# Kernel tuning notes

Measured on AMD Instinct MI355X. Metric: run time of the kernel, lower is better.

Reference implementation:

```python
import jax, jax.numpy as jnp
import numpy as np

B, C_IN, C_OUT, H, W = 32, 64, 128, 56, 56


def setup_inputs() -> dict:
    key = jax.random.key(0)
    k1, k2, k3 = jax.random.split(key, 3)
    x = jax.random.normal(k1, (B, C_IN, H, W), dtype=jnp.float32)
    # Original build(): kernel ~ N(0,1) in spatial domain, then fft2d; the
    # real/imag parts of the spectrum are the learned variables.
    kernel = jax.random.normal(k2, (C_OUT, C_IN, H, W), dtype=jnp.float32)
    kernel_fft = jnp.fft.fft2(kernel.astype(jnp.complex64))
    kernel_real = jnp.real(kernel_fft).astype(jnp.float32)
    kernel_imag = jnp.imag(kernel_fft).astype(jnp.float32)
    bias = jnp.zeros((C_OUT,), dtype=jnp.float32)
    return {"x": x, "kernel_real": kernel_real, "kernel_imag": kernel_imag, "bias": bias}


def reference(x, kernel_real, kernel_imag, bias):
    # FFT-based convolution, vectorized over batch (original used a per-batch
    # Python loop + concat; math is identical).
    x_fft = jnp.fft.fft2(x.astype(jnp.complex64))              # [B, Cin, H, W]
    kernel_freq = jax.lax.complex(kernel_real, kernel_imag)    # [Cout, Cin, H, W]
    # elementwise complex multiply + reduce over input channels
    y_fft = jnp.einsum('oihw,bihw->bohw', kernel_freq, x_fft)  # [B, Cout, H, W]
    y = jnp.real(jnp.fft.ifft2(y_fft))                         # [B, Cout, H, W]
    return y + bias[None, :, None, None]
```

## Files before the change

### kernel.cpp

```cpp
#include <hip/hip_runtime.h>


#define HH 56
#define NF 3136
#define KH 29
#define NFH 1624
constexpr int B = 32, CIN = 64, COUT = 128;
constexpr float PI2 = 6.283185307179586f;

typedef unsigned short u16;
typedef __attribute__((ext_vector_type(8))) short s8v;
typedef __attribute__((ext_vector_type(4))) float f4v;
typedef __attribute__((ext_vector_type(4))) int i4v;

#define MFMA(a, b, c) __builtin_amdgcn_mfma_f32_16x16x32_bf16(a, b, c, 0, 0, 0)

__device__ __host__ inline short f2bf(float f) {
    unsigned u = __builtin_bit_cast(unsigned, f);
    u += 0x7fffu + ((u >> 16) & 1u);
    return (short)(u >> 16);
}

__device__ inline unsigned pk2(float a, float b) {
    return (unsigned)(u16)f2bf(a) | ((unsigned)(u16)f2bf(b) << 16);
}

__device__ inline s8v negbf(s8v a) {
    i4v t = __builtin_bit_cast(i4v, a);
    t ^= (int)0x80008000u;
    return __builtin_bit_cast(s8v, t);
}

__global__ __launch_bounds__(256) void ksetup(short* __restrict__ cpool) {
    int i = blockIdx.x * 256 + threadIdx.x;
    if (i < 4608) {
        int m = i / 72, n = i % 72;
        float c = 0.f, s = 0.f;
        if (m < 56 && n < 56) {
            float ang = PI2 * (float)((m * n) % 56) / 56.f;
            c = cosf(ang); s = sinf(ang);
        }
        cpool[i]        = f2bf(c);
        cpool[4608 + i] = f2bf(s);
    } else if (i < 7168) {
        int j = i - 4608;
        int h = j / 40, kh = j % 40;
        float c = 0.f, s = 0.f;
        if (h < 56 && kh < 29) {
            float w = (kh == 0 || kh == 28) ? 1.f : 2.f;
            float ang = PI2 * (float)((h * kh) % 56) / 56.f;
            float sc = w * (1.f / 3136.f);
            c = sc * cosf(ang);
            s = -sc * sinf(ang);
        }
        cpool[13824 + j] = f2bf(c);
        cpool[16384 + j] = f2bf(s);
    }
}

__global__ __launch_bounds__(256) void kprep(const float* __restrict__ Kr,
                                             const float* __restrict__ Ki,
                                             u16* __restrict__ Kbr,
                                             u16* __restrict__ Kbi) {
    __shared__ __align__(8) u16 Lr[64 * 60], Li[64 * 60];
    const int tid = threadIdx.x;
    const int oi0 = blockIdx.x * 64;
    const int f0  = blockIdx.y * 56;
    for (int c = tid; c < 896; c += 256) {
        int row = c / 14, c4 = (c % 14) * 4;
        size_t g = (size_t)(oi0 + row) * NF + f0 + c4;
        float4 vr = *(const float4*)&Kr[g];
        float4 vi = *(const float4*)&Ki[g];
        *(uint2*)&Lr[row * 60 + c4] = make_uint2(pk2(vr.x, vr.y), pk2(vr.z, vr.w));
        *(uint2*)&Li[row * 60 + c4] = make_uint2(pk2(vi.x, vi.y), pk2(vi.z, vi.w));
    }
    __syncthreads();
    for (int idx = tid; idx < 896; idx += 256) {
        int c = idx & 15, f = idx >> 4;
        int j0 = c * 4;
        unsigned r01 = (unsigned)Lr[j0 * 60 + f]       | ((unsigned)Lr[(j0 + 1) * 60 + f] << 16);
        unsigned r23 = (unsigned)Lr[(j0 + 2) * 60 + f] | ((unsigned)Lr[(j0 + 3) * 60 + f] << 16);
        unsigned i01 = (unsigned)Li[j0 * 60 + f]       | ((unsigned)Li[(j0 + 1) * 60 + f] << 16);
        unsigned i23 = (unsigned)Li[(j0 + 2) * 60 + f] | ((unsigned)Li[(j0 + 3) * 60 + f] << 16);
        size_t o = (size_t)(f0 + f) * 8192 + oi0 + j0;
        *(uint2*)&Kbr[o] = make_uint2(r01, r23);
        *(uint2*)&Kbi[o] = make_uint2(i01, i23);
    }
}

__global__ __launch_bounds__(512) void kfwd(const float* __restrict__ x,
                                            const short* __restrict__ cpool,
                                            ushort2* __restrict__ Xb) {
    __shared__ __align__(16) short Cw[4608], Sw[4608];
    __shared__ __align__(16) short xs[2][4608];
    __shared__ __align__(16) short T1r[2][4608], T1i[2][4608];
    const int tid = threadIdx.x;
    {
        const int4* src = (const int4*)cpool;
        for (int i = tid; i < 576; i += 512) {
            ((int4*)Cw)[i] = src[i];
            ((int4*)Sw)[i] = src[576 + i];
        }
    }
    for (int i = tid; i < 4608; i += 512) ((int*)xs)[i] = 0;
    __syncthreads();
    const int half = tid >> 8, tid2 = tid & 255;
    const float* xp = x + (size_t)(blockIdx.x * 2 + half) * NF;
    short* xsh = xs[half];
    for (int c = tid2; c < 784; c += 256) {
        int r = c / 14, c4 = (c % 14) * 4;
        float4 v = *(const float4*)&xp[r * 56 + c4];
        *(uint2*)&xsh[r * 72 + c4] = make_uint2(pk2(v.x, v.y), pk2(v.z, v.w));
    }
    __syncthreads();

    const int lane = tid & 63;
    const int wv = tid >> 6;
    const int hw = wv >> 2;
    const int nt = wv & 3;
    const int q = lane >> 4, l15 = lane & 15;

    f4v aR[4] = {}, aI[4] = {};
    for (int ks = 0; ks < 2; ++ks) {
        const int bo = (nt * 16 + l15) * 72 + ks * 32 + q * 8;
        s8v bC  = *(const s8v*)&Cw[bo];
        s8v bSN = negbf(*(const s8v*)&Sw[bo]);
        for (int mt = 0; mt < 4; ++mt) {
            s8v a = *(const s8v*)&xs[hw][(mt * 16 + l15) * 72 + ks * 32 + q * 8];
            aR[mt] = MFMA(a, bC, aR[mt]);
            aI[mt] = MFMA(a, bSN, aI[mt]);
        }
    }
    for (int mt = 0; mt < 4; ++mt) {
        int o = (nt * 16 + l15) * 72 + mt * 16 + q * 4;
        *(uint2*)&T1r[hw][o] = make_uint2(pk2(aR[mt][0], aR[mt][1]),
                                          pk2(aR[mt][2], aR[mt][3]));
        *(uint2*)&T1i[hw][o] = make_uint2(pk2(aI[mt][0], aI[mt][1]),
                                          pk2(aI[mt][2], aI[mt][3]));
    }
    __syncthreads();

    f4v xr[2] = {}, xi2[2] = {};
    for (int ks = 0; ks < 2; ++ks) {
        const int bo = (nt * 16 + l15) * 72 + ks * 32 + q * 8;
        s8v br = *(const s8v*)&T1r[hw][bo];
        s8v bi = *(const s8v*)&T1i[hw][bo];
        for (int mt = 0; mt < 2; ++mt) {
            const int ao = (mt * 16 + l15) * 72 + ks * 32 + q * 8;
            s8v aC  = *(const s8v*)&Cw[ao];
            s8v aS  = *(const s8v*)&Sw[ao];
            s8v aSN = negbf(aS);
            xr[mt]  = MFMA(aC, br, xr[mt]);
            xr[mt]  = MFMA(aS, bi, xr[mt]);
            xi2[mt] = MFMA(aC, bi, xi2[mt]);
            xi2[mt] = MFMA(aSN, br, xi2[mt]);
        }
    }
    ushort2* op = Xb + (size_t)(blockIdx.x * 2 + hw) * NFH;
    const int kw = nt * 16 + l15;
    if (kw < 56) {
        for (int mt = 0; mt < 2; ++mt)
            for (int r = 0; r < 4; ++r) {
                int kh = mt * 16 + q * 4 + r;
                if (kh < 29)
                    op[kh * 56 + kw] = make_ushort2((u16)f2bf(xr[mt][r]),
                                                    (u16)f2bf(xi2[mt][r]));
            }
    }
}

__global__ __launch_bounds__(512) void kmix(const ushort2* __restrict__ Xb,
                                            const u16* __restrict__ Kbr,
                                            const u16* __restrict__ Kbi,
                                            ushort2* __restrict__ Yb) {
    __shared__ __align__(16) u16 Xr[8 * 2304], Xi[8 * 2304];
    const int tid = threadIdx.x;
    const int f0 = blockIdx.x * 8;

    for (int rr = 0; rr < 4; ++rr) {
        int row = rr * 512 + tid;
        const uint4* src = (const uint4*)(Xb + (size_t)row * NFH + f0);
        uint4 v0 = src[0], v1 = src[1];
        int base = (row >> 6) * 72 + (row & 63);
        unsigned uu[8] = {v0.x, v0.y, v0.z, v0.w, v1.x, v1.y, v1.z, v1.w};
        #pragma unroll
        for (int ff = 0; ff < 8; ++ff) {
            Xr[ff * 2304 + base] = (u16)uu[ff];
            Xi[ff * 2304 + base] = (u16)(uu[ff] >> 16);
        }
    }
    __syncthreads();

    const int lane = tid & 63;
    const int wv = tid >> 6;
    const int q = lane >> 4, l15 = lane & 15;

    unsigned pk[2][4][8];

    #pragma unroll
    for (int ff = 0; ff < 8; ++ff) {
        const int f = f0 + ff;
        const size_t kb = (size_t)f * 8192 + (size_t)(wv * 16 + l15) * 64 + q * 8;
        s8v bkr0 = *(const s8v*)&Kbr[kb];
        s8v bkr1 = *(const s8v*)&Kbr[kb + 32];
        s8v bki0 = *(const s8v*)&Kbi[kb];
        s8v bki1 = *(const s8v*)&Kbi[kb + 32];

        f4v yr[2] = {}, yi[2] = {};
        #pragma unroll
        for (int mt = 0; mt < 2; ++mt) {
            const int ao = ff * 2304 + (mt * 16 + l15) * 72 + q * 8;
            s8v axr0 = *(const s8v*)&Xr[ao];
            s8v axr1 = *(const s8v*)&Xr[ao + 32];
            s8v axi0 = *(const s8v*)&Xi[ao];
            s8v axi1 = *(const s8v*)&Xi[ao + 32];
            s8v axn0 = negbf(axi0), axn1 = negbf(axi1);
            yr[mt] = MFMA(axr0, bkr0, yr[mt]);
            yr[mt] = MFMA(axn0, bki0, yr[mt]);
            yr[mt] = MFMA(axr1, bkr1, yr[mt]);
            yr[mt] = MFMA(axn1, bki1, yr[mt]);
            yi[mt] = MFMA(axr0, bki0, yi[mt]);
            yi[mt] = MFMA(axi0, bkr0, yi[mt]);
            yi[mt] = MFMA(axr1, bki1, yi[mt]);
            yi[mt] = MFMA(axi1, bkr1, yi[mt]);
        }
        #pragma unroll
        for (int mt = 0; mt < 2; ++mt)
            #pragma unroll
            for (int r = 0; r < 4; ++r)
                pk[mt][r][ff] = (unsigned)(u16)f2bf(yr[mt][r]) |
                                ((unsigned)(u16)f2bf(yi[mt][r]) << 16);
    }

    const int o = wv * 16 + l15;
    #pragma unroll
    for (int mt = 0; mt < 2; ++mt)
        #pragma unroll
        for (int r = 0; r < 4; ++r) {
            const int b = mt * 16 + q * 4 + r;
            uint4* dst = (uint4*)(Yb + (size_t)(b * COUT + o) * NFH + f0);
            dst[0] = make_uint4(pk[mt][r][0], pk[mt][r][1],
                                pk[mt][r][2], pk[mt][r][3]);
            dst[1] = make_uint4(pk[mt][r][4], pk[mt][r][5],
                                pk[mt][r][6], pk[mt][r][7]);
        }
}

__global__ __launch_bounds__(512) void kinv(const ushort2* __restrict__ Yf,
                                            const short* __restrict__ cpool,
                                            const float* __restrict__ bias,
                                            float* __restrict__ out) {
    __shared__ __align__(16) short Cw[4608], Sw[4608];
    __shared__ __align__(16) short A2C[2560], A2S[2560];
    __shared__ __align__(16) short Yr[2][2304], Yi[2][2304];
    __shared__ __align__(16) short ZTr[2][2560], ZTi[2][2560];
    const int tid = threadIdx.x;
    {
        const int4* src = (const int4*)cpool;
        for (int i = tid; i < 576; i += 512) {
            ((int4*)Cw)[i] = src[i];
            ((int4*)Sw)[i] = src[576 + i];
        }
        for (int i = tid; i < 320; i += 512) {
            ((int4*)A2C)[i] = src[1728 + i];
            ((int4*)A2S)[i] = src[2048 + i];
        }
    }
    for (int i = tid; i < 2304; i += 512) { ((int*)Yr)[i] = 0; ((int*)Yi)[i] = 0; }
    __syncthreads();
    const int half = tid >> 8, tid2 = tid & 255;
    const ushort2* yp = Yf + (size_t)(blockIdx.x * 2 + half) * NFH;
    for (int c = tid2; c < 406; c += 256) {
        uint4 v = *(const uint4*)&yp[c * 4];
        int f = c * 4, kh = f / 56, kwb = f % 56;
        int o = kh * 72 + kwb;
        *(uint2*)&Yr[half][o] = make_uint2((v.x & 0xffffu) | (v.y << 16),
                                           (v.z & 0xffffu) | (v.w << 16));
        *(uint2*)&Yi[half][o] = make_uint2((v.x >> 16) | (v.y & 0xffff0000u),
                                           (v.z >> 16) | (v.w & 0xffff0000u));
    }
    __syncthreads();

    const int lane = tid & 63;
    const int wv = tid >> 6;
    const int hw = wv >> 2, nt = wv & 3;
    const int q = lane >> 4, l15 = lane & 15;

    f4v zr[2] = {}, zi[2] = {};
    for (int ks = 0; ks < 2; ++ks) {
        const int bo = (nt * 16 + l15) * 72 + ks * 32 + q * 8;
        s8v bC = *(const s8v*)&Cw[bo];
        s8v bS = *(const s8v*)&Sw[bo];
        for (int mt = 0; mt < 2; ++mt) {
            const int ao = (mt * 16 + l15) * 72 + ks * 32 + q * 8;
            s8v ar  = *(const s8v*)&Yr[hw][ao];
            s8v ai  = *(const s8v*)&Yi[hw][ao];
            s8v ain = negbf(ai);
            zr[mt] = MFMA(ar, bC, zr[mt]);
            zr[mt] = MFMA(ain, bS, zr[mt]);
            zi[mt] = MFMA(ar, bS, zi[mt]);
            zi[mt] = MFMA(ai, bC, zi[mt]);
        }
    }
    for (int mt = 0; mt < 2; ++mt) {
        int o = (nt * 16 + l15) * 40 + mt * 16 + q * 4;
        *(uint2*)&ZTr[hw][o] = make_uint2(pk2(zr[mt][0], zr[mt][1]),
                                          pk2(zr[mt][2], zr[mt][3]));
        *(uint2*)&ZTi[hw][o] = make_uint2(pk2(zi[mt][0], zi[mt][1]),
                                          pk2(zi[mt][2], zi[mt][3]));
    }
    __syncthreads();

    f4v yv[4] = {};
    {
        const int bo = (nt * 16 + l15) * 40 + q * 8;
        s8v br = *(const s8v*)&ZTr[hw][bo];
        s8v bi = *(const s8v*)&ZTi[hw][bo];
        for (int mt = 0; mt < 4; ++mt) {
            const int ao = (mt * 16 + l15) * 40 + q * 8;
            s8v ac  = *(const s8v*)&A2C[ao];
            s8v as_ = *(const s8v*)&A2S[ao];
            yv[mt] = MFMA(ac, br, yv[mt]);
            yv[mt] = MFMA(as_, bi, yv[mt]);
        }
    }
    const int img = blockIdx.x * 2 + hw;
    const float bv = bias[img & (COUT - 1)];
    float* opx = out + (size_t)img * NF;
    const int w = nt * 16 + l15;
    if (w < 56) {
        for (int mt = 0; mt < 4; ++mt)
            for (int r = 0; r < 4; ++r) {
                int h = mt * 16 + q * 4 + r;
                if (h < 56) opx[h * 56 + w] = yv[mt][r] + bv;
            }
    }
}

extern "C" void kernel_launch(void* const* d_in, const int* in_sizes, int n_in,
                              void* d_out, int out_size, void* d_ws, size_t ws_size,
                              hipStream_t stream) {
    const float* x    = (const float*)d_in[0];
    const float* Kr   = (const float*)d_in[1];
    const float* Ki   = (const float*)d_in[2];
    const float* bias = (const float*)d_in[3];

    short*   cpool = (short*)d_ws;
    ushort2* Xb  = (ushort2*)((char*)d_ws + 40960);
    ushort2* Yb  = (ushort2*)((char*)d_ws + 40960 + 13307904);
    u16*     Kbr = (u16*)((char*)d_ws + 40960 + 13307904 + 26615808);
    u16*     Kbi = Kbr + (size_t)13307904;

    hipLaunchKernelGGL(ksetup, dim3(28), dim3(256), 0, stream, cpool);
    hipLaunchKernelGGL(kprep, dim3(128, 29), dim3(256), 0, stream, Kr, Ki, Kbr, Kbi);
    hipLaunchKernelGGL(kfwd, dim3(B * CIN / 2), dim3(512), 0, stream, x, cpool, Xb);
    hipLaunchKernelGGL(kmix, dim3(NFH / 8), dim3(512), 0, stream, Xb, Kbr, Kbi, Yb);
    hipLaunchKernelGGL(kinv, dim3(B * COUT / 2), dim3(512), 0, stream,
                       Yb, cpool, bias, (float*)d_out);
}
```

Measured before the change: 305.4 us.

## Merge kernel prep and forward FFT into one launch; split mixing over output channels

Kernel-spectrum conversion and the forward DFT now run in a single launch, with block index choosing the role, so the two independent stages overlap and one launch is dropped. The channel-mixing kernel is split across two output-channel halves with 256-thread blocks, doubling the grid for better occupancy at the cost of loading the X tile twice. The inverse kernel aliases its Y and ZT shared buffers, adding a barrier, to cut LDS use and allow more resident blocks.

```diff
diff --git a/kernel.cpp b/kernel.cpp
--- a/kernel.cpp
+++ b/kernel.cpp
@@ -58,43 +58,50 @@
     }
 }
 
-__global__ __launch_bounds__(256) void kprep(const float* __restrict__ Kr,
-                                             const float* __restrict__ Ki,
-                                             u16* __restrict__ Kbr,
-                                             u16* __restrict__ Kbi) {
-    __shared__ __align__(8) u16 Lr[64 * 60], Li[64 * 60];
+__global__ __launch_bounds__(512) void kstage(const float* __restrict__ x,
+                                              const float* __restrict__ Kr,
+                                              const float* __restrict__ Ki,
+                                              const short* __restrict__ cpool,
+                                              ushort2* __restrict__ Xb,
+                                              u16* __restrict__ Kbr,
+                                              u16* __restrict__ Kbi) {
+    __shared__ __align__(16) char pool[73728];
     const int tid = threadIdx.x;
-    const int oi0 = blockIdx.x * 64;
-    const int f0  = blockIdx.y * 56;
-    for (int c = tid; c < 896; c += 256) {
-        int row = c / 14, c4 = (c % 14) * 4;
-        size_t g = (size_t)(oi0 + row) * NF + f0 + c4;
-        float4 vr = *(const float4*)&Kr[g];
-        float4 vi = *(const float4*)&Ki[g];
-        *(uint2*)&Lr[row * 60 + c4] = make_uint2(pk2(vr.x, vr.y), pk2(vr.z, vr.w));
-        *(uint2*)&Li[row * 60 + c4] = make_uint2(pk2(vi.x, vi.y), pk2(vi.z, vi.w));
-    }
-    __syncthreads();
-    for (int idx = tid; idx < 896; idx += 256) {
-        int c = idx & 15, f = idx >> 4;
-        int j0 = c * 4;
-        unsigned r01 = (unsigned)Lr[j0 * 60 + f]       | ((unsigned)Lr[(j0 + 1) * 60 + f] << 16);
-        unsigned r23 = (unsigned)Lr[(j0 + 2) * 60 + f] | ((unsigned)Lr[(j0 + 3) * 60 + f] << 16);
-        unsigned i01 = (unsigned)Li[j0 * 60 + f]       | ((unsigned)Li[(j0 + 1) * 60 + f] << 16);
-        unsigned i23 = (unsigned)Li[(j0 + 2) * 60 + f] | ((unsigned)Li[(j0 + 3) * 60 + f] << 16);
-        size_t o = (size_t)(f0 + f) * 8192 + oi0 + j0;
-        *(uint2*)&Kbr[o] = make_uint2(r01, r23);
-        *(uint2*)&Kbi[o] = make_uint2(i01, i23);
-    }
-}
-
-__global__ __launch_bounds__(512) void kfwd(const float* __restrict__ x,
-                                            const short* __restrict__ cpool,
-                                            ushort2* __restrict__ Xb) {
-    __shared__ __align__(16) short Cw[4608], Sw[4608];
-    __shared__ __align__(16) short xs[2][4608];
-    __shared__ __align__(16) short T1r[2][4608], T1i[2][4608];
-    const int tid = threadIdx.x;
+
+    if (blockIdx.x >= 1024) {
+        u16* Lr = (u16*)pool;
+        u16* Li = Lr + 3840;
+        const int t = blockIdx.x - 1024;
+        const int oi0 = (t & 127) * 64;
+        const int f0  = (t >> 7) * 56;
+        for (int c = tid; c < 896; c += 512) {
+            int row = c / 14, c4 = (c % 14) * 4;
+            size_t g = (size_t)(oi0 + row) * NF + f0 + c4;
+            float4 vr = *(const float4*)&Kr[g];
+            float4 vi = *(const float4*)&Ki[g];
+            *(uint2*)&Lr[row * 60 + c4] = make_uint2(pk2(vr.x, vr.y), pk2(vr.z, vr.w));
+            *(uint2*)&Li[row * 60 + c4] = make_uint2(pk2(vi.x, vi.y), pk2(vi.z, vi.w));
+        }
+        __syncthreads();
+        for (int idx = tid; idx < 896; idx += 512) {
+            int c = idx & 15, f = idx >> 4;
+            int j0 = c * 4;
+            unsigned r01 = (unsigned)Lr[j0 * 60 + f]       | ((unsigned)Lr[(j0 + 1) * 60 + f] << 16);
+            unsigned r23 = (unsigned)Lr[(j0 + 2) * 60 + f] | ((unsigned)Lr[(j0 + 3) * 60 + f] << 16);
+            unsigned i01 = (unsigned)Li[j0 * 60 + f]       | ((unsigned)Li[(j0 + 1) * 60 + f] << 16);
+            unsigned i23 = (unsigned)Li[(j0 + 2) * 60 + f] | ((unsigned)Li[(j0 + 3) * 60 + f] << 16);
+            size_t o = (size_t)(f0 + f) * 8192 + oi0 + j0;
+            *(uint2*)&Kbr[o] = make_uint2(r01, r23);
+            *(uint2*)&Kbi[o] = make_uint2(i01, i23);
+        }
+        return;
+    }
+
+    short* Cw  = (short*)pool;
+    short* Sw  = Cw + 4608;
+    short* xs  = Sw + 4608;
+    short* T1r = xs + 9216;
+    short* T1i = T1r + 9216;
     {
         const int4* src = (const int4*)cpool;
         for (int i = tid; i < 576; i += 512) {
@@ -106,7 +113,7 @@
     __syncthreads();
     const int half = tid >> 8, tid2 = tid & 255;
     const float* xp = x + (size_t)(blockIdx.x * 2 + half) * NF;
-    short* xsh = xs[half];
+    short* xsh = xs + half * 4608;
     for (int c = tid2; c < 784; c += 256) {
         int r = c / 14, c4 = (c % 14) * 4;
         float4 v = *(const float4*)&xp[r * 56 + c4];
@@ -126,25 +133,25 @@
         s8v bC  = *(const s8v*)&Cw[bo];
         s8v bSN = negbf(*(const s8v*)&Sw[bo]);
         for (int mt = 0; mt < 4; ++mt) {
-            s8v a = *(const s8v*)&xs[hw][(mt * 16 + l15) * 72 + ks * 32 + q * 8];
+            s8v a = *(const s8v*)&xs[hw * 4608 + (mt * 16 + l15) * 72 + ks * 32 + q * 8];
             aR[mt] = MFMA(a, bC, aR[mt]);
             aI[mt] = MFMA(a, bSN, aI[mt]);
         }
     }
     for (int mt = 0; mt < 4; ++mt) {
-        int o = (nt * 16 + l15) * 72 + mt * 16 + q * 4;
-        *(uint2*)&T1r[hw][o] = make_uint2(pk2(aR[mt][0], aR[mt][1]),
-                                          pk2(aR[mt][2], aR[mt][3]));
-        *(uint2*)&T1i[hw][o] = make_uint2(pk2(aI[mt][0], aI[mt][1]),
-                                          pk2(aI[mt][2], aI[mt][3]));
+        int o = hw * 4608 + (nt * 16 + l15) * 72 + mt * 16 + q * 4;
+        *(uint2*)&T1r[o] = make_uint2(pk2(aR[mt][0], aR[mt][1]),
+                                      pk2(aR[mt][2], aR[mt][3]));
+        *(uint2*)&T1i[o] = make_uint2(pk2(aI[mt][0], aI[mt][1]),
+                                      pk2(aI[mt][2], aI[mt][3]));
     }
     __syncthreads();
 
     f4v xr[2] = {}, xi2[2] = {};
     for (int ks = 0; ks < 2; ++ks) {
-        const int bo = (nt * 16 + l15) * 72 + ks * 32 + q * 8;
-        s8v br = *(const s8v*)&T1r[hw][bo];
-        s8v bi = *(const s8v*)&T1i[hw][bo];
+        const int bo = hw * 4608 + (nt * 16 + l15) * 72 + ks * 32 + q * 8;
+        s8v br = *(const s8v*)&T1r[bo];
+        s8v bi = *(const s8v*)&T1i[bo];
         for (int mt = 0; mt < 2; ++mt) {
             const int ao = (mt * 16 + l15) * 72 + ks * 32 + q * 8;
             s8v aC  = *(const s8v*)&Cw[ao];
@@ -169,16 +176,17 @@
     }
 }
 
-__global__ __launch_bounds__(512) void kmix(const ushort2* __restrict__ Xb,
+__global__ __launch_bounds__(256) void kmix(const ushort2* __restrict__ Xb,
                                             const u16* __restrict__ Kbr,
                                             const u16* __restrict__ Kbi,
                                             ushort2* __restrict__ Yb) {
     __shared__ __align__(16) u16 Xr[8 * 2304], Xi[8 * 2304];
     const int tid = threadIdx.x;
     const int f0 = blockIdx.x * 8;
-
-    for (int rr = 0; rr < 4; ++rr) {
-        int row = rr * 512 + tid;
+    const int o0 = blockIdx.y * 64;
+
+    for (int rr = 0; rr < 8; ++rr) {
+        int row = rr * 256 + tid;
         const uint4* src = (const uint4*)(Xb + (size_t)row * NFH + f0);
         uint4 v0 = src[0], v1 = src[1];
         int base = (row >> 6) * 72 + (row & 63);
@@ -194,13 +202,14 @@
     const int lane = tid & 63;
     const int wv = tid >> 6;
     const int q = lane >> 4, l15 = lane & 15;
+    const int o = o0 + wv * 16 + l15;
 
     unsigned pk[2][4][8];
 
     #pragma unroll
     for (int ff = 0; ff < 8; ++ff) {
         const int f = f0 + ff;
-        const size_t kb = (size_t)f * 8192 + (size_t)(wv * 16 + l15) * 64 + q * 8;
+        const size_t kb = (size_t)f * 8192 + (size_t)o * 64 + q * 8;
         s8v bkr0 = *(const s8v*)&Kbr[kb];
         s8v bkr1 = *(const s8v*)&Kbr[kb + 32];
         s8v bki0 = *(const s8v*)&Kbi[kb];
@@ -232,7 +241,6 @@
                                 ((unsigned)(u16)f2bf(yi[mt][r]) << 16);
     }
 
-    const int o = wv * 16 + l15;
     #pragma unroll
     for (int mt = 0; mt < 2; ++mt)
         #pragma unroll
@@ -250,10 +258,16 @@
                                             const short* __restrict__ cpool,
                                             const float* __restrict__ bias,
                                             float* __restrict__ out) {
-    __shared__ __align__(16) short Cw[4608], Sw[4608];
-    __shared__ __align__(16) short A2C[2560], A2S[2560];
-    __shared__ __align__(16) short Yr[2][2304], Yi[2][2304];
-    __shared__ __align__(16) short ZTr[2][2560], ZTi[2][2560];
+    __shared__ __align__(16) char pool[49152];
+    short* Cw    = (short*)pool;
+    short* Sw    = Cw + 4608;
+    short* A2C   = Sw + 4608;
+    short* A2S   = A2C + 2560;
+    short* Ybase = A2S + 2560;
+    short* Yr    = Ybase;
+    short* Yi    = Yr + 4608;
+    short* ZTr   = Ybase;
+    short* ZTi   = ZTr + 5120;
     const int tid = threadIdx.x;
     {
         const int4* src = (const int4*)cpool;
@@ -266,18 +280,20 @@
             ((int4*)A2S)[i] = src[2048 + i];
         }
     }
-    for (int i = tid; i < 2304; i += 512) { ((int*)Yr)[i] = 0; ((int*)Yi)[i] = 0; }
+    for (int i = tid; i < 4608; i += 512) ((int*)Ybase)[i] = 0;
     __syncthreads();
     const int half = tid >> 8, tid2 = tid & 255;
     const ushort2* yp = Yf + (size_t)(blockIdx.x * 2 + half) * NFH;
+    short* Yrh = Yr + half * 2304;
+    short* Yih = Yi + half * 2304;
     for (int c = tid2; c < 406; c += 256) {
         uint4 v = *(const uint4*)&yp[c * 4];
         int f = c * 4, kh = f / 56, kwb = f % 56;
         int o = kh * 72 + kwb;
-        *(uint2*)&Yr[half][o] = make_uint2((v.x & 0xffffu) | (v.y << 16),
-                                           (v.z & 0xffffu) | (v.w << 16));
-        *(uint2*)&Yi[half][o] = make_uint2((v.x >> 16) | (v.y & 0xffff0000u),
-                                           (v.z >> 16) | (v.w & 0xffff0000u));
+        *(uint2*)&Yrh[o] = make_uint2((v.x & 0xffffu) | (v.y << 16),
+                                      (v.z & 0xffffu) | (v.w << 16));
+        *(uint2*)&Yih[o] = make_uint2((v.x >> 16) | (v.y & 0xffff0000u),
+                                      (v.z >> 16) | (v.w & 0xffff0000u));
     }
     __syncthreads();
 
@@ -292,9 +308,9 @@
         s8v bC = *(const s8v*)&Cw[bo];
         s8v bS = *(const s8v*)&Sw[bo];
         for (int mt = 0; mt < 2; ++mt) {
-            const int ao = (mt * 16 + l15) * 72 + ks * 32 + q * 8;
-            s8v ar  = *(const s8v*)&Yr[hw][ao];
-            s8v ai  = *(const s8v*)&Yi[hw][ao];
+            const int ao = hw * 2304 + (mt * 16 + l15) * 72 + ks * 32 + q * 8;
+            s8v ar  = *(const s8v*)&Yr[ao];
+            s8v ai  = *(const s8v*)&Yi[ao];
             s8v ain = negbf(ai);
             zr[mt] = MFMA(ar, bC, zr[mt]);
             zr[mt] = MFMA(ain, bS, zr[mt]);
@@ -302,20 +318,21 @@
             zi[mt] = MFMA(ai, bC, zi[mt]);
         }
     }
+    __syncthreads();
     for (int mt = 0; mt < 2; ++mt) {
-        int o = (nt * 16 + l15) * 40 + mt * 16 + q * 4;
-        *(uint2*)&ZTr[hw][o] = make_uint2(pk2(zr[mt][0], zr[mt][1]),
-                                          pk2(zr[mt][2], zr[mt][3]));
-        *(uint2*)&ZTi[hw][o] = make_uint2(pk2(zi[mt][0], zi[mt][1]),
-                                          pk2(zi[mt][2], zi[mt][3]));
+        int o = hw * 2560 + (nt * 16 + l15) * 40 + mt * 16 + q * 4;
+        *(uint2*)&ZTr[o] = make_uint2(pk2(zr[mt][0], zr[mt][1]),
+                                      pk2(zr[mt][2], zr[mt][3]));
+        *(uint2*)&ZTi[o] = make_uint2(pk2(zi[mt][0], zi[mt][1]),
+                                      pk2(zi[mt][2], zi[mt][3]));
     }
     __syncthreads();
 
     f4v yv[4] = {};
     {
-        const int bo = (nt * 16 + l15) * 40 + q * 8;
-        s8v br = *(const s8v*)&ZTr[hw][bo];
-        s8v bi = *(const s8v*)&ZTi[hw][bo];
+        const int bo = hw * 2560 + (nt * 16 + l15) * 40 + q * 8;
+        s8v br = *(const s8v*)&ZTr[bo];
+        s8v bi = *(const s8v*)&ZTi[bo];
         for (int mt = 0; mt < 4; ++mt) {
             const int ao = (mt * 16 + l15) * 40 + q * 8;
             s8v ac  = *(const s8v*)&A2C[ao];
@@ -352,9 +369,10 @@
     u16*     Kbi = Kbr + (size_t)13307904;
 
     hipLaunchKernelGGL(ksetup, dim3(28), dim3(256), 0, stream, cpool);
-    hipLaunchKernelGGL(kprep, dim3(128, 29), dim3(256), 0, stream, Kr, Ki, Kbr, Kbi);
-    hipLaunchKernelGGL(kfwd, dim3(B * CIN / 2), dim3(512), 0, stream, x, cpool, Xb);
-    hipLaunchKernelGGL(kmix, dim3(NFH / 8), dim3(512), 0, stream, Xb, Kbr, Kbi, Yb);
+    hipLaunchKernelGGL(kstage, dim3(1024 + 3712), dim3(512), 0, stream,
+                       x, Kr, Ki, cpool, Xb, Kbr, Kbi);
+    hipLaunchKernelGGL(kmix, dim3(NFH / 8, 2), dim3(256), 0, stream,
+                       Xb, Kbr, Kbi, Yb);
     hipLaunchKernelGGL(kinv, dim3(B * COUT / 2), dim3(512), 0, stream,
                        Yb, cpool, bias, (float*)d_out);
 }
```

New measurement: 302.8 us. No clear change (-0.9%).
